# Optimization experiments

Measured on AMD Instinct MI355X. Metric: run time of the kernel, lower is better.

Reference implementation:

```python
import jax, jax.numpy as jnp
import numpy as np

B, TQ, TK, D, F, H = 16, 256, 256, 256, 36, 8
DK = D // H          # dk = d // h
SF = int(np.sqrt(F)) # 6
MASK_VALUE = -1e30


def setup_inputs() -> dict:
    rng = jax.random.key(0)
    ks = jax.random.split(rng, 12)
    s = 0.05
    return {
        "query": jax.random.normal(ks[0], (B, TQ, D), jnp.float32),
        "key_ts": jax.random.normal(ks[1], (B, TK, D), jnp.float32),
        "value": jax.random.normal(ks[2], (B, TK, F), jnp.float32),
        "mask": (jax.random.uniform(ks[3], (B, TK, F)) < 0.5).astype(jnp.float32),
        "Wq": jax.random.normal(ks[4], (H, D, DK), jnp.float32) * s,
        "Wk": jax.random.normal(ks[5], (H, D, DK), jnp.float32) * s,
        "Wc": jax.random.normal(ks[6], (H, D), jnp.float32) * s,
        "bc": jnp.zeros((D,), jnp.float32),
        "Wo_1": jax.random.normal(ks[7], (F, SF), jnp.float32) * s,
        "bo_1": jnp.zeros((SF,), jnp.float32),
        "Wo_2": jax.random.normal(ks[8], (SF, 1), jnp.float32) * s,
        "bo_2": jnp.zeros((D,), jnp.float32),
    }


def reference(query, key_ts, value, mask, Wq, Wk, Wc, bc, Wo_1, bo_1, Wo_2, bo_2):
    # mask: [B, Tk, F] 0/1 missingness indicator -> broadcast as [B, 1, Tk, F]
    m = mask[:, None, :, :]
    heads = []
    for j in range(Wq.shape[0]):  # fixed small head loop (h=8)
        q = query @ Wq[j]                                  # [B, Tq, dk]
        k = key_ts @ Wk[j]                                 # [B, Tk, dk]
        A = jnp.einsum('bqd,bkd->bqk', q, k)[..., None]    # [B, Tq, Tk, 1] (no 1/sqrt(dk) scaling, as in original)
        A = m * A + (1.0 - m) * MASK_VALUE                 # [B, Tq, Tk, F]
        A = jax.nn.softmax(A, axis=-2)                     # softmax over Tk, per feature
        heads.append(jnp.einsum('bqkf,bkf->bqf', A, value))  # masked weighted sum
    latent = jnp.stack(heads, axis=-1)                     # [B, Tq, F, h]
    # permute (0,2,1,3) -> [B, F, Tq, h]; dot Wc[h,d] -> [B, F, Tq, d]
    latent = jnp.tanh(jnp.einsum('bqfh,hd->bfqd', latent, Wc) + bc)
    # permute (0,2,3,1) -> [B, Tq, d, F]; Wo_1: F -> sqrt(F)
    x = jnp.tanh(jnp.einsum('bfqd,fs->bqds', latent, Wo_1) + bo_1)
    # Wo_2: sqrt(F) -> 1, squeeze, add bo_2 -> [B, Tq, d]
    x = jnp.einsum('bqds,so->bqd', x, Wo_2) + bo_2
    return x
```

## Files before the change

kernel.cpp:

```cpp
#include <hip/hip_runtime.h>

#define NB 16
#define NTQ 256
#define NTK 256
#define ND 256
#define NF 36
#define NH 8
#define NDK 32
#define NSF 6

typedef __attribute__((ext_vector_type(8))) short short8;
typedef __attribute__((ext_vector_type(4))) float f32x4;
#define MFMA16(a,b,c) __builtin_amdgcn_mfma_f32_16x16x32_bf16(a,b,c,0,0,0)

#define SZ_QP  (16*8*256*32*2)
#define QPH_OFF 0
#define QPL_OFF (QPH_OFF + SZ_QP)
#define KPH_OFF (QPL_OFF + SZ_QP)
#define KPL_OFF (KPH_OFF + SZ_QP)
#define SZ_RT  (16*80*256*2)
#define RT_OFF  (KPL_OFF + SZ_QP)
#define HD_OFF  (RT_OFF + SZ_RT)

__device__ __forceinline__ short f2bf(float x){
    union { float f; unsigned u; } v; v.f = x;
    unsigned r = v.u + 0x7fffu + ((v.u >> 16) & 1u);
    return (short)(r >> 16);
}
__device__ __forceinline__ float bf2f(short s){
    union { float f; unsigned u; } v; v.u = ((unsigned)(unsigned short)s) << 16;
    return v.f;
}
__device__ __forceinline__ float fast_tanh(float x){
    float e = __expf(2.0f*x);
    return 1.0f - 2.0f/(e + 1.0f);
}
__device__ __forceinline__ short8 ld8(const short* p){ return *(const short8*)p; }

__device__ __forceinline__ void cvt8(const float* __restrict__ p, short8& h8, short8& l8){
    f32x4 a = *(const f32x4*)p;
    f32x4 c = *(const f32x4*)(p + 4);
    #pragma unroll
    for (int i = 0; i < 4; ++i){
        short h0 = f2bf(a[i]); h8[i]   = h0; l8[i]   = f2bf(a[i] - bf2f(h0));
        short h1 = f2bf(c[i]); h8[4+i] = h1; l8[4+i] = f2bf(c[i] - bf2f(h1));
    }
}

__global__ void imta_prep(const float* __restrict__ query, const float* __restrict__ key_ts,
                          const float* __restrict__ Wq, const float* __restrict__ Wk,
                          const float* __restrict__ mask, const float* __restrict__ value,
                          char* __restrict__ wsb){
    if (blockIdx.y == 2){
        const int b = blockIdx.z, k = threadIdx.x;
        short* rt = (short*)(wsb + RT_OFF) + b*80*256;
        #pragma unroll
        for (int r = 0; r < 5; ++r){
            const int fp = blockIdx.x*5 + r;
            const int f = fp >> 1;
            short o = 0;
            if (f < NF){
                float m = mask[(b*NTK + k)*NF + f];
                o = (fp & 1) ? f2bf(m) : f2bf(m * value[(b*NTK + k)*NF + f]);
            }
            rt[fp*256 + k] = o;
        }
        return;
    }
    const int side = blockIdx.y, b = blockIdx.z;
    const int mt = blockIdx.x >> 1, nh = blockIdx.x & 1;
    const int t0 = mt*32;
    const int tid = threadIdx.x, w = tid >> 6, lane = tid & 63;
    const int col = lane & 15, quad = lane >> 4;
    const float* __restrict__ X = side ? key_ts : query;
    const float* __restrict__ W = side ? Wk : Wq;
    __shared__ float sX[32][36];
    __shared__ float sW[128][36];
    const int xr = tid >> 3, xc = (tid & 7)*4;
    const int dr = tid >> 3, dkq = (tid & 7)*4;
    f32x4 acc[2][2];
    #pragma unroll
    for (int m = 0; m < 2; ++m){ acc[m][0] = (f32x4)0.f; acc[m][1] = (f32x4)0.f; }
    for (int kb = 0; kb < 8; ++kb){
        const int dc = kb*32;
        float4 xv = *(const float4*)(X + (size_t)(b*NTQ + t0 + xr)*ND + dc + xc);
        float4 wv[4];
        #pragma unroll
        for (int jj = 0; jj < 4; ++jj)
            wv[jj] = *(const float4*)(W + (size_t)((4*nh + jj)*ND + dc + dr)*NDK + dkq);
        __syncthreads();
        *(float4*)&sX[xr][xc] = xv;
        #pragma unroll
        for (int jj = 0; jj < 4; ++jj)
            #pragma unroll
            for (int i = 0; i < 4; ++i)
                sW[jj*32 + dkq + i][dr] = ((const float*)&wv[jj])[i];
        __syncthreads();
        short8 ah[2], al[2], bh[2], bl[2];
        #pragma unroll
        for (int m = 0; m < 2; ++m)
            cvt8(&sX[m*16 + col][quad*8], ah[m], al[m]);
        #pragma unroll
        for (int nt = 0; nt < 2; ++nt)
            cvt8(&sW[(w*2 + nt)*16 + col][quad*8], bh[nt], bl[nt]);
        #pragma unroll
        for (int m = 0; m < 2; ++m)
            #pragma unroll
            for (int nt = 0; nt < 2; ++nt){
                acc[m][nt] = MFMA16(al[m], bh[nt], acc[m][nt]);
                acc[m][nt] = MFMA16(ah[m], bl[nt], acc[m][nt]);
                acc[m][nt] = MFMA16(ah[m], bh[nt], acc[m][nt]);
            }
    }
    short* oh = (short*)(wsb + (side ? KPH_OFF : QPH_OFF));
    short* ol = (short*)(wsb + (side ? KPL_OFF : QPL_OFF));
    #pragma unroll
    for (int m = 0; m < 2; ++m)
        #pragma unroll
        for (int nt = 0; nt < 2; ++nt){
            const int n = (nh*8 + w*2 + nt)*16 + col;
            const int j = n >> 5, dk = n & 31;
            #pragma unroll
            for (int r = 0; r < 4; ++r){
                const int t = t0 + m*16 + quad*4 + r;
                float v = acc[m][nt][r];
                short h = f2bf(v);
                size_t o = (size_t)(((b*NH + j)*NTQ + t)*NDK + dk);
                oh[o] = h; ol[o] = f2bf(v - bf2f(h));
            }
        }
}

__global__ void imta_attn(char* __restrict__ wsb, const float* __restrict__ value){
    const int t0 = blockIdx.x*64;
    const int j = blockIdx.y, b = blockIdx.z;
    const int tid = threadIdx.x, w = tid >> 6, lane = tid & 63;
    const int col = lane & 15, quad = lane >> 4;
    __shared__ short sE[64*264];
    const short* QH = (const short*)(wsb + QPH_OFF) + (b*NH + j)*NTQ*NDK;
    const short* QL = (const short*)(wsb + QPL_OFF) + (b*NH + j)*NTQ*NDK;
    const short* KH = (const short*)(wsb + KPH_OFF) + (b*NH + j)*NTK*NDK;
    const short* KL = (const short*)(wsb + KPL_OFF) + (b*NH + j)*NTK*NDK;
    const short* RT = (const short*)(wsb + RT_OFF) + b*80*256;
    float* HD = (float*)(wsb + HD_OFF) + (b*NH + j)*NTQ*NF;

    short8 ah[4], al[4];
    #pragma unroll
    for (int m = 0; m < 4; ++m){
        const int t = t0 + m*16 + col;
        ah[m] = ld8(QH + t*NDK + quad*8);
        al[m] = ld8(QL + t*NDK + quad*8);
    }
    #pragma unroll
    for (int nt = 0; nt < 4; ++nt){
        const int key0 = w*64 + nt*16;
        short8 bh = ld8(KH + (key0 + col)*NDK + quad*8);
        short8 bl = ld8(KL + (key0 + col)*NDK + quad*8);
        f32x4 acc[4];
        #pragma unroll
        for (int m = 0; m < 4; ++m){
            f32x4 c = (f32x4)0.f;
            c = MFMA16(al[m], bh, c);
            c = MFMA16(ah[m], bl, c);
            c = MFMA16(ah[m], bh, c);
            acc[m] = c;
        }
        const int key = key0 + col;
        #pragma unroll
        for (int m = 0; m < 4; ++m)
            #pragma unroll
            for (int r = 0; r < 4; ++r){
                const int q = m*16 + quad*4 + r;
                sE[q*264 + key] = f2bf(__expf(acc[m][r]));
            }
    }
    __syncthreads();

    const int q0 = w*16;
    f32x4 acc2[5];
    #pragma unroll
    for (int nt = 0; nt < 5; ++nt) acc2[nt] = (f32x4)0.f;
    #pragma unroll 2
    for (int kb = 0; kb < 8; ++kb){
        const int ko = kb*32 + quad*8;
        short8 a = *(const short8*)&sE[(q0 + col)*264 + ko];
        #pragma unroll
        for (int nt = 0; nt < 5; ++nt){
            short8 bb = ld8(RT + (nt*16 + col)*256 + ko);
            acc2[nt] = MFMA16(a, bb, acc2[nt]);
        }
    }
    __syncthreads();
    float* sH = (float*)sE;
    #pragma unroll
    for (int nt = 0; nt < 5; ++nt)
        #pragma unroll
        for (int r = 0; r < 4; ++r){
            float v = acc2[nt][r];
            float o = __shfl_xor(v, 1, 64);
            if (!(col & 1)){
                const int f = nt*8 + (col >> 1);
                if (f < NF){
                    float num = v, den = o, h;
                    if (den != 0.0f) h = num/den;
                    else {
                        float s = 0.f;
                        for (int k = 0; k < NTK; ++k) s += value[(b*NTK + k)*NF + f];
                        h = s * (1.0f/256.0f);
                    }
                    sH[(q0 + quad*4 + r)*40 + f] = h;
                }
            }
        }
    __syncthreads();
    for (int idx = tid; idx < 64*NF; idx += 256){
        const int q = idx/NF, f = idx - q*NF;
        HD[(t0 + q)*NF + f] = sH[q*40 + f];
    }
}

__global__ void imta_final(const float* __restrict__ Wc, const float* __restrict__ bc,
                           const float* __restrict__ Wo1, const float* __restrict__ bo1,
                           const float* __restrict__ Wo2, const float* __restrict__ bo2,
                           const float* __restrict__ hd, float* __restrict__ out){
    const int bq = blockIdx.x;
    const int b = bq >> 8, qq = bq & 255;
    const int tid = threadIdx.x;
    __shared__ float sh[NF*NH];
    __shared__ float sW1[NF*NSF];
    for (int t = tid; t < NF*NH; t += 256){
        int jj = t/NF, f = t - jj*NF;
        sh[t] = hd[((b*NH + jj)*NTQ + qq)*NF + f];
    }
    if (tid < NF*NSF) sW1[tid] = Wo1[tid];
    __syncthreads();
    const int d = tid;
    float wcr[8];
    #pragma unroll
    for (int h = 0; h < 8; ++h) wcr[h] = Wc[h*ND + d];
    const float bcd = bc[d];
    float a2[6];
    #pragma unroll
    for (int s = 0; s < 6; ++s) a2[s] = bo1[s];
    #pragma unroll
    for (int f4 = 0; f4 < NF; f4 += 4){
        float4 sv[8];
        #pragma unroll
        for (int h = 0; h < 8; ++h) sv[h] = *(const float4*)&sh[h*NF + f4];
        #pragma unroll
        for (int fi = 0; fi < 4; ++fi){
            float a = bcd;
            #pragma unroll
            for (int h = 0; h < 8; ++h)
                a = fmaf(reinterpret_cast<const float*>(&sv[h])[fi], wcr[h], a);
            float lf = fast_tanh(a);
            const int f = f4 + fi;
            #pragma unroll
            for (int s = 0; s < 6; ++s)
                a2[s] = fmaf(lf, sW1[f*NSF + s], a2[s]);
        }
    }
    float o = bo2[d];
    #pragma unroll
    for (int s = 0; s < 6; ++s)
        o = fmaf(fast_tanh(a2[s]), Wo2[s], o);
    out[(b*NTQ + qq)*ND + d] = o;
}

extern "C" void kernel_launch(void* const* d_in, const int* in_sizes, int n_in,
                              void* d_out, int out_size, void* d_ws, size_t ws_size,
                              hipStream_t stream){
    const float* query  = (const float*)d_in[0];
    const float* key_ts = (const float*)d_in[1];
    const float* value  = (const float*)d_in[2];
    const float* mask   = (const float*)d_in[3];
    const float* Wq     = (const float*)d_in[4];
    const float* Wk     = (const float*)d_in[5];
    const float* Wc     = (const float*)d_in[6];
    const float* bc     = (const float*)d_in[7];
    const float* Wo1    = (const float*)d_in[8];
    const float* bo1    = (const float*)d_in[9];
    const float* Wo2    = (const float*)d_in[10];
    const float* bo2    = (const float*)d_in[11];
    char* wsb  = (char*)d_ws;
    float* out = (float*)d_out;
    (void)in_sizes; (void)n_in; (void)out_size; (void)ws_size;

    imta_prep <<<dim3(16, 3, 16), dim3(256), 0, stream>>>(query, key_ts, Wq, Wk, mask, value, wsb);
    imta_attn <<<dim3(4, 8, 16),  dim3(256), 0, stream>>>(wsb, value);
    imta_final<<<dim3(4096),      dim3(256), 0, stream>>>(Wc, bc, Wo1, bo1, Wo2, bo2,
                                                          (const float*)(wsb + HD_OFF), out);
}
```

Measured before the change: 142.4 us.

## Fuse attention and output-projection kernels via a device-wide atomic grid barrier

After: 196.9 us. +38.3%, slower.

```diff
diff --git a/kernel.cpp b/kernel.cpp
--- a/kernel.cpp
+++ b/kernel.cpp
@@ -21,6 +21,7 @@
 #define SZ_RT  (16*80*256*2)
 #define RT_OFF  (KPL_OFF + SZ_QP)
 #define HD_OFF  (RT_OFF + SZ_RT)
+#define CTR_OFF (HD_OFF + 16*8*256*36*4)
 
 __device__ __forceinline__ short f2bf(float x){
     union { float f; unsigned u; } v; v.f = x;
@@ -53,6 +54,8 @@
                           char* __restrict__ wsb){
     if (blockIdx.y == 2){
         const int b = blockIdx.z, k = threadIdx.x;
+        if (blockIdx.x == 0 && b == 0 && k == 0)
+            *(unsigned*)(wsb + CTR_OFF) = 0u;
         short* rt = (short*)(wsb + RT_OFF) + b*80*256;
         #pragma unroll
         for (int r = 0; r < 5; ++r){
@@ -131,7 +134,12 @@
         }
 }
 
-__global__ void imta_attn(char* __restrict__ wsb, const float* __restrict__ value){
+__global__ void __launch_bounds__(256, 2)
+imta_attn_final(char* __restrict__ wsb, const float* __restrict__ value,
+                const float* __restrict__ Wc, const float* __restrict__ bc,
+                const float* __restrict__ Wo1, const float* __restrict__ bo1,
+                const float* __restrict__ Wo2, const float* __restrict__ bo2,
+                float* __restrict__ out){
     const int t0 = blockIdx.x*64;
     const int j = blockIdx.y, b = blockIdx.z;
     const int tid = threadIdx.x, w = tid >> 6, lane = tid & 63;
@@ -142,7 +150,8 @@
     const short* KH = (const short*)(wsb + KPH_OFF) + (b*NH + j)*NTK*NDK;
     const short* KL = (const short*)(wsb + KPL_OFF) + (b*NH + j)*NTK*NDK;
     const short* RT = (const short*)(wsb + RT_OFF) + b*80*256;
-    float* HD = (float*)(wsb + HD_OFF) + (b*NH + j)*NTQ*NF;
+    float* HDall = (float*)(wsb + HD_OFF);
+    float* HD = HDall + (b*NH + j)*NTQ*NF;
 
     short8 ah[4], al[4];
     #pragma unroll
@@ -217,54 +226,67 @@
         const int q = idx/NF, f = idx - q*NF;
         HD[(t0 + q)*NF + f] = sH[q*40 + f];
     }
-}
-
-__global__ void imta_final(const float* __restrict__ Wc, const float* __restrict__ bc,
-                           const float* __restrict__ Wo1, const float* __restrict__ bo1,
-                           const float* __restrict__ Wo2, const float* __restrict__ bo2,
-                           const float* __restrict__ hd, float* __restrict__ out){
-    const int bq = blockIdx.x;
-    const int b = bq >> 8, qq = bq & 255;
-    const int tid = threadIdx.x;
-    __shared__ float sh[NF*NH];
-    __shared__ float sW1[NF*NSF];
-    for (int t = tid; t < NF*NH; t += 256){
-        int jj = t/NF, f = t - jj*NF;
-        sh[t] = hd[((b*NH + jj)*NTQ + qq)*NF + f];
-    }
+
+    {
+        unsigned* ctr = (unsigned*)(wsb + CTR_OFF);
+        __syncthreads();
+        if (tid == 0){
+            __threadfence();
+            atomicAdd(ctr, 1u);
+            while (atomicAdd(ctr, 0u) < 512u)
+                __builtin_amdgcn_s_sleep(8);
+            __threadfence();
+        }
+        __syncthreads();
+    }
+
+    float* sh  = (float*)sE;
+    float* sW1 = (float*)sE + 320;
     if (tid < NF*NSF) sW1[tid] = Wo1[tid];
-    __syncthreads();
     const int d = tid;
     float wcr[8];
     #pragma unroll
     for (int h = 0; h < 8; ++h) wcr[h] = Wc[h*ND + d];
-    const float bcd = bc[d];
-    float a2[6];
-    #pragma unroll
-    for (int s = 0; s < 6; ++s) a2[s] = bo1[s];
-    #pragma unroll
-    for (int f4 = 0; f4 < NF; f4 += 4){
-        float4 sv[8];
-        #pragma unroll
-        for (int h = 0; h < 8; ++h) sv[h] = *(const float4*)&sh[h*NF + f4];
-        #pragma unroll
-        for (int fi = 0; fi < 4; ++fi){
-            float a = bcd;
-            #pragma unroll
-            for (int h = 0; h < 8; ++h)
-                a = fmaf(reinterpret_cast<const float*>(&sv[h])[fi], wcr[h], a);
-            float lf = fast_tanh(a);
-            const int f = f4 + fi;
-            #pragma unroll
-            for (int s = 0; s < 6; ++s)
-                a2[s] = fmaf(lf, sW1[f*NSF + s], a2[s]);
-        }
-    }
-    float o = bo2[d];
-    #pragma unroll
-    for (int s = 0; s < 6; ++s)
-        o = fmaf(fast_tanh(a2[s]), Wo2[s], o);
-    out[(b*NTQ + qq)*ND + d] = o;
+    const float bcd = bc[d], bod = bo2[d];
+    float b1[6], w2[6];
+    #pragma unroll
+    for (int s = 0; s < 6; ++s){ b1[s] = bo1[s]; w2[s] = Wo2[s]; }
+    const int qbase = blockIdx.x*64 + j*8;
+    for (int r = 0; r < 8; ++r){
+        const int q = qbase + r;
+        __syncthreads();
+        for (int t = tid; t < NF*NH; t += 256){
+            int jj = t/NF, f = t - jj*NF;
+            sh[t] = HDall[((b*NH + jj)*NTQ + q)*NF + f];
+        }
+        __syncthreads();
+        float a2[6];
+        #pragma unroll
+        for (int s = 0; s < 6; ++s) a2[s] = b1[s];
+        #pragma unroll
+        for (int f4 = 0; f4 < NF; f4 += 4){
+            float4 sv[8];
+            #pragma unroll
+            for (int h = 0; h < 8; ++h) sv[h] = *(const float4*)&sh[h*NF + f4];
+            #pragma unroll
+            for (int fi = 0; fi < 4; ++fi){
+                float a = bcd;
+                #pragma unroll
+                for (int h = 0; h < 8; ++h)
+                    a = fmaf(reinterpret_cast<const float*>(&sv[h])[fi], wcr[h], a);
+                float lf = fast_tanh(a);
+                const int f = f4 + fi;
+                #pragma unroll
+                for (int s = 0; s < 6; ++s)
+                    a2[s] = fmaf(lf, sW1[f*NSF + s], a2[s]);
+            }
+        }
+        float o = bod;
+        #pragma unroll
+        for (int s = 0; s < 6; ++s)
+            o = fmaf(fast_tanh(a2[s]), w2[s], o);
+        out[(b*NTQ + q)*ND + d] = o;
+    }
 }
 
 extern "C" void kernel_launch(void* const* d_in, const int* in_sizes, int n_in,
@@ -286,8 +308,8 @@
     float* out = (float*)d_out;
     (void)in_sizes; (void)n_in; (void)out_size; (void)ws_size;
 
-    imta_prep <<<dim3(16, 3, 16), dim3(256), 0, stream>>>(query, key_ts, Wq, Wk, mask, value, wsb);
-    imta_attn <<<dim3(4, 8, 16),  dim3(256), 0, stream>>>(wsb, value);
-    imta_final<<<dim3(4096),      dim3(256), 0, stream>>>(Wc, bc, Wo1, bo1, Wo2, bo2,
-                                                          (const float*)(wsb + HD_OFF), out);
-}
+    imta_prep      <<<dim3(16, 3, 16), dim3(256), 0, stream>>>(query, key_ts, Wq, Wk,
+                                                               mask, value, wsb);
+    imta_attn_final<<<dim3(4, 8, 16),  dim3(256), 0, stream>>>(wsb, value, Wc, bc,
+                                                               Wo1, bo1, Wo2, bo2, out);
+}
```

## Halve attention query tile to double blocks; batch four rows per final block

Applied to the files above, without the earlier changes.

Result: slower. 226.8 us (+59.2%).

```diff
diff --git a/kernel.cpp b/kernel.cpp
--- a/kernel.cpp
+++ b/kernel.cpp
@@ -132,11 +132,11 @@
 }
 
 __global__ void imta_attn(char* __restrict__ wsb, const float* __restrict__ value){
-    const int t0 = blockIdx.x*64;
+    const int t0 = blockIdx.x*32;
     const int j = blockIdx.y, b = blockIdx.z;
     const int tid = threadIdx.x, w = tid >> 6, lane = tid & 63;
     const int col = lane & 15, quad = lane >> 4;
-    __shared__ short sE[64*264];
+    __shared__ short sE[32*264];
     const short* QH = (const short*)(wsb + QPH_OFF) + (b*NH + j)*NTQ*NDK;
     const short* QL = (const short*)(wsb + QPL_OFF) + (b*NH + j)*NTQ*NDK;
     const short* KH = (const short*)(wsb + KPH_OFF) + (b*NH + j)*NTK*NDK;
@@ -144,9 +144,9 @@
     const short* RT = (const short*)(wsb + RT_OFF) + b*80*256;
     float* HD = (float*)(wsb + HD_OFF) + (b*NH + j)*NTQ*NF;
 
-    short8 ah[4], al[4];
-    #pragma unroll
-    for (int m = 0; m < 4; ++m){
+    short8 ah[2], al[2];
+    #pragma unroll
+    for (int m = 0; m < 2; ++m){
         const int t = t0 + m*16 + col;
         ah[m] = ld8(QH + t*NDK + quad*8);
         al[m] = ld8(QL + t*NDK + quad*8);
@@ -156,9 +156,9 @@
         const int key0 = w*64 + nt*16;
         short8 bh = ld8(KH + (key0 + col)*NDK + quad*8);
         short8 bl = ld8(KL + (key0 + col)*NDK + quad*8);
-        f32x4 acc[4];
-        #pragma unroll
-        for (int m = 0; m < 4; ++m){
+        f32x4 acc[2];
+        #pragma unroll
+        for (int m = 0; m < 2; ++m){
             f32x4 c = (f32x4)0.f;
             c = MFMA16(al[m], bh, c);
             c = MFMA16(ah[m], bl, c);
@@ -167,7 +167,7 @@
         }
         const int key = key0 + col;
         #pragma unroll
-        for (int m = 0; m < 4; ++m)
+        for (int m = 0; m < 2; ++m)
             #pragma unroll
             for (int r = 0; r < 4; ++r){
                 const int q = m*16 + quad*4 + r;
@@ -176,44 +176,48 @@
     }
     __syncthreads();
 
-    const int q0 = w*16;
-    f32x4 acc2[5];
-    #pragma unroll
-    for (int nt = 0; nt < 5; ++nt) acc2[nt] = (f32x4)0.f;
+    const int q0 = (w & 1)*16;
+    const int ntbase = (w >> 1) ? 3 : 0;
+    const int ntcnt  = (w >> 1) ? 2 : 3;
+    f32x4 acc2[3];
+    #pragma unroll
+    for (int t = 0; t < 3; ++t) acc2[t] = (f32x4)0.f;
     #pragma unroll 2
     for (int kb = 0; kb < 8; ++kb){
         const int ko = kb*32 + quad*8;
         short8 a = *(const short8*)&sE[(q0 + col)*264 + ko];
         #pragma unroll
-        for (int nt = 0; nt < 5; ++nt){
-            short8 bb = ld8(RT + (nt*16 + col)*256 + ko);
-            acc2[nt] = MFMA16(a, bb, acc2[nt]);
-        }
+        for (int t = 0; t < 3; ++t)
+            if (t < ntcnt){
+                short8 bb = ld8(RT + ((ntbase + t)*16 + col)*256 + ko);
+                acc2[t] = MFMA16(a, bb, acc2[t]);
+            }
     }
     __syncthreads();
     float* sH = (float*)sE;
     #pragma unroll
-    for (int nt = 0; nt < 5; ++nt)
-        #pragma unroll
-        for (int r = 0; r < 4; ++r){
-            float v = acc2[nt][r];
-            float o = __shfl_xor(v, 1, 64);
-            if (!(col & 1)){
-                const int f = nt*8 + (col >> 1);
-                if (f < NF){
-                    float num = v, den = o, h;
-                    if (den != 0.0f) h = num/den;
-                    else {
-                        float s = 0.f;
-                        for (int k = 0; k < NTK; ++k) s += value[(b*NTK + k)*NF + f];
-                        h = s * (1.0f/256.0f);
+    for (int t = 0; t < 3; ++t)
+        if (t < ntcnt)
+            #pragma unroll
+            for (int r = 0; r < 4; ++r){
+                float v = acc2[t][r];
+                float o = __shfl_xor(v, 1, 64);
+                if (!(col & 1)){
+                    const int f = (ntbase + t)*8 + (col >> 1);
+                    if (f < NF){
+                        float num = v, den = o, h;
+                        if (den != 0.0f) h = num/den;
+                        else {
+                            float s = 0.f;
+                            for (int k = 0; k < NTK; ++k) s += value[(b*NTK + k)*NF + f];
+                            h = s * (1.0f/256.0f);
+                        }
+                        sH[(q0 + quad*4 + r)*40 + f] = h;
                     }
-                    sH[(q0 + quad*4 + r)*40 + f] = h;
                 }
             }
-        }
     __syncthreads();
-    for (int idx = tid; idx < 64*NF; idx += 256){
+    for (int idx = tid; idx < 32*NF; idx += 256){
         const int q = idx/NF, f = idx - q*NF;
         HD[(t0 + q)*NF + f] = sH[q*40 + f];
     }
@@ -223,14 +227,14 @@
                            const float* __restrict__ Wo1, const float* __restrict__ bo1,
                            const float* __restrict__ Wo2, const float* __restrict__ bo2,
                            const float* __restrict__ hd, float* __restrict__ out){
-    const int bq = blockIdx.x;
-    const int b = bq >> 8, qq = bq & 255;
+    const int b = blockIdx.x >> 6, q0 = (blockIdx.x & 63)*4;
     const int tid = threadIdx.x;
-    __shared__ float sh[NF*NH];
+    __shared__ float sh[4*NF*NH];
     __shared__ float sW1[NF*NSF];
-    for (int t = tid; t < NF*NH; t += 256){
-        int jj = t/NF, f = t - jj*NF;
-        sh[t] = hd[((b*NH + jj)*NTQ + qq)*NF + f];
+    for (int t = tid; t < 4*NF*NH; t += 256){
+        int r = t/(NF*NH), rem = t - r*(NF*NH);
+        int jj = rem/NF, f = rem - jj*NF;
+        sh[t] = hd[((b*NH + jj)*NTQ + q0 + r)*NF + f];
     }
     if (tid < NF*NSF) sW1[tid] = Wo1[tid];
     __syncthreads();
@@ -238,33 +242,39 @@
     float wcr[8];
     #pragma unroll
     for (int h = 0; h < 8; ++h) wcr[h] = Wc[h*ND + d];
-    const float bcd = bc[d];
-    float a2[6];
-    #pragma unroll
-    for (int s = 0; s < 6; ++s) a2[s] = bo1[s];
-    #pragma unroll
-    for (int f4 = 0; f4 < NF; f4 += 4){
-        float4 sv[8];
-        #pragma unroll
-        for (int h = 0; h < 8; ++h) sv[h] = *(const float4*)&sh[h*NF + f4];
-        #pragma unroll
-        for (int fi = 0; fi < 4; ++fi){
-            float a = bcd;
-            #pragma unroll
-            for (int h = 0; h < 8; ++h)
-                a = fmaf(reinterpret_cast<const float*>(&sv[h])[fi], wcr[h], a);
-            float lf = fast_tanh(a);
-            const int f = f4 + fi;
-            #pragma unroll
-            for (int s = 0; s < 6; ++s)
-                a2[s] = fmaf(lf, sW1[f*NSF + s], a2[s]);
+    const float bcd = bc[d], bod = bo2[d];
+    float b1[6], w2[6];
+    #pragma unroll
+    for (int s = 0; s < 6; ++s){ b1[s] = bo1[s]; w2[s] = Wo2[s]; }
+    for (int r = 0; r < 4; ++r){
+        const float* __restrict__ shr = &sh[r*NF*NH];
+        float a2[6];
+        #pragma unroll
+        for (int s = 0; s < 6; ++s) a2[s] = b1[s];
+        #pragma unroll
+        for (int f4 = 0; f4 < NF; f4 += 4){
+            float4 sv[8];
+            #pragma unroll
+            for (int h = 0; h < 8; ++h) sv[h] = *(const float4*)&shr[h*NF + f4];
+            #pragma unroll
+            for (int fi = 0; fi < 4; ++fi){
+                float a = bcd;
+                #pragma unroll
+                for (int h = 0; h < 8; ++h)
+                    a = fmaf(reinterpret_cast<const float*>(&sv[h])[fi], wcr[h], a);
+                float lf = fast_tanh(a);
+                const int f = f4 + fi;
+                #pragma unroll
+                for (int s = 0; s < 6; ++s)
+                    a2[s] = fmaf(lf, sW1[f*NSF + s], a2[s]);
+            }
         }
-    }
-    float o = bo2[d];
-    #pragma unroll
-    for (int s = 0; s < 6; ++s)
-        o = fmaf(fast_tanh(a2[s]), Wo2[s], o);
-    out[(b*NTQ + qq)*ND + d] = o;
+        float o = bod;
+        #pragma unroll
+        for (int s = 0; s < 6; ++s)
+            o = fmaf(fast_tanh(a2[s]), w2[s], o);
+        out[(b*NTQ + q0 + r)*ND + d] = o;
+    }
 }
 
 extern "C" void kernel_launch(void* const* d_in, const int* in_sizes, int n_in,
@@ -286,8 +296,9 @@
     float* out = (float*)d_out;
     (void)in_sizes; (void)n_in; (void)out_size; (void)ws_size;
 
-    imta_prep <<<dim3(16, 3, 16), dim3(256), 0, stream>>>(query, key_ts, Wq, Wk, mask, value, wsb);
-    imta_attn <<<dim3(4, 8, 16),  dim3(256), 0, stream>>>(wsb, value);
-    imta_final<<<dim3(4096),      dim3(256), 0, stream>>>(Wc, bc, Wo1, bo1, Wo2, bo2,
+    imta_prep <<<dim3(16, 3, 16), dim3(256), 0, stream>>>(query, key_ts, Wq, Wk,
+                                                          mask, value, wsb);
+    imta_attn <<<dim3(8, 8, 16),  dim3(256), 0, stream>>>(wsb, value);
+    imta_final<<<dim3(1024),      dim3(256), 0, stream>>>(Wc, bc, Wo1, bo1, Wo2, bo2,
                                                           (const float*)(wsb + HD_OFF), out);
 }
```
